# Optimization experiments

Hardware: AMD Instinct MI355X
Metric: run time of the kernel (lower is better)

The kernel has to match this reference:

```python
import jax
import jax.numpy as jnp
from jax import lax
import numpy as np

N_BITS = 24
OUT_BITS = 48
BATCH = 131072

# Shift tensor: S[i, j, i+j] = 1, used to place partial product i (24 bits)
# into a 48-bit lane shifted left by i (LSB-first layout).
_ii, _jj = np.meshgrid(np.arange(N_BITS), np.arange(N_BITS), indexing='ij')
_S = np.zeros((N_BITS, N_BITS, OUT_BITS), dtype=np.float32)
_S[_ii, _jj, _ii + _jj] = 1.0
SHIFT = jnp.asarray(_S)


def bit_add(a, b):
    """Ripple-carry binary adder on LSB-first bit vectors.
    a, b: [..., 48] with entries in {0,1}. Returns sum bits [..., 48]
    (carry out of bit 47 is discarded; 24x24 product never overflows 48 bits)."""
    a_t = jnp.moveaxis(a, -1, 0)  # [48, ...]
    b_t = jnp.moveaxis(b, -1, 0)

    def step(carry, ab):
        ai, bi = ab
        t = ai + bi + carry          # 0..3
        s = jnp.mod(t, 2.0)          # sum bit (XOR of three inputs)
        c = jnp.floor(t * 0.5)       # majority carry
        return c, s

    c0 = jnp.zeros(a_t.shape[1:], dtype=a.dtype)
    _, s = lax.scan(step, c0, (a_t, b_t))
    return jnp.moveaxis(s, 0, -1)


def reference(A, B):
    """A, B: [..., 24] LSB-first bits -> product bits [..., 48] LSB-first."""
    # Partial products: pp[i, j] = B_i AND A_j (AND == product for {0,1} spikes)
    M = B[..., :, None] * A[..., None, :]                 # [..., 24(i), 24(j)]
    # Zero-pad/shift each row i left by i bits into 48-bit lanes
    pp = jnp.einsum('...ij,ijk->...ik', M, SHIFT)         # [..., 24, 48]
    pps = jnp.moveaxis(pp, -2, 0)                         # [24, ..., 48]

    # Parallel (tree) accumulation, O(log n) adder levels: 24->12->6->3->2->1
    while pps.shape[0] > 1:
        n = pps.shape[0]
        even = pps[: (n // 2) * 2]
        summed = bit_add(even[0::2], even[1::2])
        if n % 2 == 1:
            summed = jnp.concatenate([summed, pps[-1:]], axis=0)
        pps = summed
    return pps[0]


def setup_inputs() -> dict:
    key = jax.random.key(0)
    kA, kB = jax.random.split(key)
    A = jax.random.randint(kA, (BATCH, N_BITS), 0, 2).astype(jnp.float32)
    B = jax.random.randint(kB, (BATCH, N_BITS), 0, 2).astype(jnp.float32)
    return {"A": A, "B": B}
```

## Files before the change

kernel.cpp:

```cpp
#include <hip/hip_runtime.h>
#include <stdint.h>


#define NBATCH 131072
#define N_BITS 24
#define OUT_BITS 48

__global__ __launch_bounds__(256) void ArrayMultiplier24x24_kernel(
    const float* __restrict__ A,
    const float* __restrict__ B,
    float* __restrict__ out)
{
    int i = blockIdx.x * blockDim.x + threadIdx.x;
    if (i >= NBATCH) return;

    const float4* a4 = reinterpret_cast<const float4*>(A + (size_t)i * N_BITS);
    const float4* b4 = reinterpret_cast<const float4*>(B + (size_t)i * N_BITS);

    uint32_t a = 0u, b = 0u;
#pragma unroll
    for (int q = 0; q < 6; ++q) {
        float4 va = a4[q];
        float4 vb = b4[q];
        int s = 4 * q;
        a |= ((uint32_t)va.x) << (s + 0);
        a |= ((uint32_t)va.y) << (s + 1);
        a |= ((uint32_t)va.z) << (s + 2);
        a |= ((uint32_t)va.w) << (s + 3);
        b |= ((uint32_t)vb.x) << (s + 0);
        b |= ((uint32_t)vb.y) << (s + 1);
        b |= ((uint32_t)vb.z) << (s + 2);
        b |= ((uint32_t)vb.w) << (s + 3);
    }

    uint64_t p = (uint64_t)a * (uint64_t)b;

    float4* o4 = reinterpret_cast<float4*>(out + (size_t)i * OUT_BITS);
#pragma unroll
    for (int q = 0; q < 12; ++q) {
        int s = 4 * q;
        float4 v;
        v.x = (float)((uint32_t)(p >> (s + 0)) & 1u);
        v.y = (float)((uint32_t)(p >> (s + 1)) & 1u);
        v.z = (float)((uint32_t)(p >> (s + 2)) & 1u);
        v.w = (float)((uint32_t)(p >> (s + 3)) & 1u);
        o4[q] = v;
    }
}

extern "C" void kernel_launch(void* const* d_in, const int* in_sizes, int n_in,
                              void* d_out, int out_size, void* d_ws, size_t ws_size,
                              hipStream_t stream)
{
    const float* A = (const float*)d_in[0];
    const float* B = (const float*)d_in[1];
    float* out = (float*)d_out;

    const int threads = 256;
    const int blocks = (NBATCH + threads - 1) / threads;
    ArrayMultiplier24x24_kernel<<<blocks, threads, 0, stream>>>(A, B, out);
}
```

Baseline: 82.00 us.

## Coalesce loads and stores through shared-memory staging with float bit-pattern packing

Reorganizes the kernel so each block loads its rows' inputs with fully coalesced 16-byte loads and extracts bit values from the float exponent bit pattern instead of float-to-int conversion. Nibbles are staged in LDS, packed per row, then output float4s are written in coalesced order, with each thread recomputing the row's product. This targets strided per-thread global accesses, at the cost of two block barriers, extra LDS traffic and redundant multiplies. The packing assumes inputs are exactly 0.0 or 1.0.

```diff
diff --git a/kernel.cpp b/kernel.cpp
--- a/kernel.cpp
+++ b/kernel.cpp
@@ -3,48 +3,59 @@
 
 
 #define NBATCH 131072
-#define N_BITS 24
-#define OUT_BITS 48
+#define RPB    256
+#define NF4IN  (RPB * 6)
 
 __global__ __launch_bounds__(256) void ArrayMultiplier24x24_kernel(
-    const float* __restrict__ A,
-    const float* __restrict__ B,
-    float* __restrict__ out)
+    const uint4* __restrict__ A4,
+    const uint4* __restrict__ B4,
+    float4* __restrict__ O4)
 {
-    int i = blockIdx.x * blockDim.x + threadIdx.x;
-    if (i >= NBATCH) return;
+    __shared__ uint32_t nibA[NF4IN];
+    __shared__ uint32_t nibB[NF4IN];
+    __shared__ uint32_t packA[RPB];
+    __shared__ uint32_t packB[RPB];
 
-    const float4* a4 = reinterpret_cast<const float4*>(A + (size_t)i * N_BITS);
-    const float4* b4 = reinterpret_cast<const float4*>(B + (size_t)i * N_BITS);
+    const int t = threadIdx.x;
+    const size_t inBase  = (size_t)blockIdx.x * NF4IN;
+    const size_t outBase = (size_t)blockIdx.x * (RPB * 12);
+
+#pragma unroll
+    for (int k = 0; k < 6; ++k) {
+        int f = k * 256 + t;
+        uint4 va = A4[inBase + f];
+        uint4 vb = B4[inBase + f];
+        uint32_t na = ((va.x >> 29) & 1u) | ((va.y >> 28) & 2u) |
+                      ((va.z >> 27) & 4u) | ((va.w >> 26) & 8u);
+        uint32_t nb = ((vb.x >> 29) & 1u) | ((vb.y >> 28) & 2u) |
+                      ((vb.z >> 27) & 4u) | ((vb.w >> 26) & 8u);
+        nibA[f] = na;
+        nibB[f] = nb;
+    }
+    __syncthreads();
 
     uint32_t a = 0u, b = 0u;
 #pragma unroll
-    for (int q = 0; q < 6; ++q) {
-        float4 va = a4[q];
-        float4 vb = b4[q];
-        int s = 4 * q;
-        a |= ((uint32_t)va.x) << (s + 0);
-        a |= ((uint32_t)va.y) << (s + 1);
-        a |= ((uint32_t)va.z) << (s + 2);
-        a |= ((uint32_t)va.w) << (s + 3);
-        b |= ((uint32_t)vb.x) << (s + 0);
-        b |= ((uint32_t)vb.y) << (s + 1);
-        b |= ((uint32_t)vb.z) << (s + 2);
-        b |= ((uint32_t)vb.w) << (s + 3);
+    for (int s = 0; s < 6; ++s) {
+        a |= nibA[t * 6 + s] << (4 * s);
+        b |= nibB[t * 6 + s] << (4 * s);
     }
+    packA[t] = a;
+    packB[t] = b;
+    __syncthreads();
 
-    uint64_t p = (uint64_t)a * (uint64_t)b;
-
-    float4* o4 = reinterpret_cast<float4*>(out + (size_t)i * OUT_BITS);
 #pragma unroll
-    for (int q = 0; q < 12; ++q) {
-        int s = 4 * q;
+    for (int k = 0; k < 12; ++k) {
+        int g = k * 256 + t;
+        int row = g / 12;
+        int c0 = (g - row * 12) * 4;
+        uint64_t p = (uint64_t)packA[row] * (uint64_t)packB[row];
         float4 v;
-        v.x = (float)((uint32_t)(p >> (s + 0)) & 1u);
-        v.y = (float)((uint32_t)(p >> (s + 1)) & 1u);
-        v.z = (float)((uint32_t)(p >> (s + 2)) & 1u);
-        v.w = (float)((uint32_t)(p >> (s + 3)) & 1u);
-        o4[q] = v;
+        v.x = (float)((uint32_t)(p >> (c0 + 0)) & 1u);
+        v.y = (float)((uint32_t)(p >> (c0 + 1)) & 1u);
+        v.z = (float)((uint32_t)(p >> (c0 + 2)) & 1u);
+        v.w = (float)((uint32_t)(p >> (c0 + 3)) & 1u);
+        O4[outBase + g] = v;
     }
 }
 
@@ -52,11 +63,10 @@
                               void* d_out, int out_size, void* d_ws, size_t ws_size,
                               hipStream_t stream)
 {
-    const float* A = (const float*)d_in[0];
-    const float* B = (const float*)d_in[1];
-    float* out = (float*)d_out;
+    const uint4* A4 = (const uint4*)d_in[0];
+    const uint4* B4 = (const uint4*)d_in[1];
+    float4* O4 = (float4*)d_out;
 
-    const int threads = 256;
-    const int blocks = (NBATCH + threads - 1) / threads;
-    ArrayMultiplier24x24_kernel<<<blocks, threads, 0, stream>>>(A, B, out);
+    const int blocks = NBATCH / RPB;
+    ArrayMultiplier24x24_kernel<<<blocks, 256, 0, stream>>>(A4, B4, O4);
 }
```

Result: faster. 76.66 us (-6.5%).
